# Kernel tuning notes

Measured on AMD Instinct MI355X. Metric: run time of the kernel, lower is better.

## Reference

```python
import jax, jax.numpy as jnp
import numpy as np
import math

TOP_K = 2
CAP_FACTOR = 1.25
AUX_W = 0.01


def setup_inputs() -> dict:
    key = jax.random.key(0)
    k1, k2 = jax.random.split(key)
    x = jax.random.normal(k1, (8192, 4096), dtype=jnp.float32)
    # gate weight, torch init std=0.01, stored as (E, D) like nn.Linear
    gate_w = jax.random.normal(k2, (64, 4096), dtype=jnp.float32) * 0.01
    return {"x": x, "gate_w": gate_w}


def reference(x, gate_w):
    N, D = x.shape
    E = gate_w.shape[0]
    K = TOP_K
    C = max(math.ceil(CAP_FACTOR * N / E), 1)  # expert capacity

    logits = x @ gate_w.T                      # (N, E)
    probs = jax.nn.softmax(logits, axis=-1)    # (N, E)
    vals, idx = jax.lax.top_k(probs, K)        # (N, K)
    vals = vals / vals.sum(axis=-1, keepdims=True)

    # Parallel replacement of the serial double loop: flatten (N,K) row-major
    # (token-major, then k) which matches the loop iteration order exactly.
    flat_e = idx.reshape(-1)                               # (N*K,) expert ids
    oh = jax.nn.one_hot(flat_e, E, dtype=jnp.int32)        # (N*K, E)
    # exclusive prefix count of prior assignments to each expert
    pos = jnp.cumsum(oh, axis=0) - oh                      # (N*K, E)
    slot = jnp.take_along_axis(pos, flat_e[:, None], axis=1)[:, 0]  # (N*K,)
    # In the torch loop the counter saturates at C (only incremented when
    # c < C), so slot==prior_total is equivalent: kept iff prior_total < C.
    keep = slot < C
    slot_s = jnp.where(keep, slot, 0)
    tok = jnp.arange(N * K) // K

    combine_weights = jnp.zeros((N, E, C), dtype=x.dtype).at[
        tok, flat_e, slot_s].add(jnp.where(keep, vals.reshape(-1), 0.0))
    dispatch_mask = (jnp.zeros((N, E, C), dtype=jnp.int32).at[
        tok, flat_e, slot_s].add(keep.astype(jnp.int32))) > 0

    # load balancing loss
    f = oh.astype(jnp.float32).reshape(N, K, E).mean(axis=(0, 1))  # (E,)
    p = probs.mean(axis=0)                                         # (E,)
    load_loss = AUX_W * E * jnp.sum(f * p)

    return dispatch_mask, combine_weights, probs, load_loss
```

## Files before the change

kernel.cpp:

```cpp
#include <hip/hip_runtime.h>
#include <math.h>

#define N_TOK 8192
#define DIM   4096
#define NEXP  64
#define CAP   160
#define NEC   (83886080ULL)
#define OFF_CW    (83886080ULL)
#define OFF_PROBS (167772160ULL)
#define OFF_LOSS  (168296448ULL)
#define NA    16384

__device__ __forceinline__ float wave_max64(float v) {
    for (int m = 1; m < 64; m <<= 1) v = fmaxf(v, __shfl_xor(v, m, 64));
    return v;
}
__device__ __forceinline__ float wave_sum64(float v) {
    for (int m = 1; m < 64; m <<= 1) v += __shfl_xor(v, m, 64);
    return v;
}
__device__ __forceinline__ void wave_argmax64(float& v, int& i) {
    for (int m = 1; m < 64; m <<= 1) {
        float ov = __shfl_xor(v, m, 64);
        int   oi = __shfl_xor(i, m, 64);
        if (ov > v || (ov == v && oi < i)) { v = ov; i = oi; }
    }
}

__global__ __launch_bounds__(256) void k_gemm(const float* __restrict__ x,
                                              const float* __restrict__ gw,
                                              float* __restrict__ part, int dps) {
    __shared__ float xs[64][68];
    __shared__ float wsh[64][68];
    const int tb = blockIdx.x * 64;
    const int d_begin = blockIdx.y * dps;
    const int t  = threadIdx.x;
    const int tx = t & 15, ty = t >> 4;
    float acc[4][4] = {};
    for (int ci = 0; ci < dps / 64; ++ci) {
        const int d0 = d_begin + ci * 64;
        for (int it = 0; it < 4; ++it) {
            int idx = t + 256 * it;
            int row = idx >> 4;
            int d4  = idx & 15;
            *(float4*)(&xs[row][4 * d4]) =
                *(const float4*)(x + (size_t)(tb + row) * DIM + d0 + 4 * d4);
            *(float4*)(&wsh[row][4 * d4]) =
                *(const float4*)(gw + (size_t)row * DIM + d0 + 4 * d4);
        }
        __syncthreads();
        for (int d4 = 0; d4 < 16; ++d4) {
            float4 xa[4], wb[4];
            for (int i = 0; i < 4; ++i) xa[i] = *(const float4*)(&xs[ty + 16 * i][4 * d4]);
            for (int j = 0; j < 4; ++j) wb[j] = *(const float4*)(&wsh[tx + 16 * j][4 * d4]);
            for (int i = 0; i < 4; ++i)
                for (int j = 0; j < 4; ++j) {
                    acc[i][j] = fmaf(xa[i].x, wb[j].x, acc[i][j]);
                    acc[i][j] = fmaf(xa[i].y, wb[j].y, acc[i][j]);
                    acc[i][j] = fmaf(xa[i].z, wb[j].z, acc[i][j]);
                    acc[i][j] = fmaf(xa[i].w, wb[j].w, acc[i][j]);
                }
        }
        __syncthreads();
    }
    for (int i = 0; i < 4; ++i)
        for (int j = 0; j < 4; ++j)
            part[(size_t)blockIdx.y * N_TOK * NEXP +
                 (size_t)(tb + ty + 16 * i) * NEXP + (tx + 16 * j)] = acc[i][j];
}

__global__ __launch_bounds__(256) void k_router(const float* __restrict__ part, int S,
                                                float* __restrict__ probs_out,
                                                int* __restrict__ rec_e,
                                                float* __restrict__ rec_w) {
    const int tok  = blockIdx.x * 4 + (threadIdx.x >> 6);
    const int lane = threadIdx.x & 63;
    float l = 0.f;
    for (int s = 0; s < S; ++s)
        l += part[(size_t)s * N_TOK * NEXP + (size_t)tok * NEXP + lane];
    const float m  = wave_max64(l);
    const float ex = expf(l - m);
    const float sm = wave_sum64(ex);
    const float p  = ex / sm;
    probs_out[(size_t)tok * NEXP + lane] = p;
    float v1 = p; int i1 = lane;
    wave_argmax64(v1, i1);
    float v2 = (lane == i1) ? -1.f : p; int i2 = lane;
    wave_argmax64(v2, i2);
    if (lane == 0) {
        const float denom = v1 + v2;
        rec_e[2 * tok]     = i1;
        rec_e[2 * tok + 1] = i2;
        rec_w[2 * tok]     = v1 / denom;
        rec_w[2 * tok + 1] = v2 / denom;
    }
}

__global__ __launch_bounds__(256) void k_preduce(const float* __restrict__ probs,
                                                 float* __restrict__ p_sum) {
    __shared__ float sh[256];
    const int e = threadIdx.x & 63, tg = threadIdx.x >> 6;
    const int tok0 = blockIdx.x * 1024;
    float a = 0.f;
    for (int k = 0; k < 256; ++k)
        a += probs[(size_t)(tok0 + tg + 4 * k) * NEXP + e];
    sh[threadIdx.x] = a;
    __syncthreads();
    if (threadIdx.x < 64) {
        float s = sh[threadIdx.x] + sh[64 + threadIdx.x] +
                  sh[128 + threadIdx.x] + sh[192 + threadIdx.x];
        atomicAdd(&p_sum[threadIdx.x], s);
    }
}

__global__ void k_count(const int* __restrict__ rec_e, int* __restrict__ chunk_cnt) {
    __shared__ int cnt[64];
    const int lane = threadIdx.x, b = blockIdx.x;
    cnt[lane] = 0;
    __syncthreads();
    for (int r = 0; r < 4; ++r)
        atomicAdd(&cnt[rec_e[b * 256 + r * 64 + lane]], 1);
    __syncthreads();
    chunk_cnt[b * 64 + lane] = cnt[lane];
}

__global__ void k_scan(const int* __restrict__ chunk_cnt, int* __restrict__ chunk_base,
                       const float* __restrict__ p_sum, float* __restrict__ loss_out) {
    const int e = threadIdx.x;
    int run = 0;
    for (int b = 0; b < 64; ++b) {
        chunk_base[b * 64 + e] = run;
        run += chunk_cnt[b * 64 + e];
    }
    float term = ((float)run / (float)NA) * (p_sum[e] / (float)N_TOK);
    term = wave_sum64(term);
    if (e == 0) loss_out[0] = 0.01f * 64.f * term;
}

__global__ void k_slots(const int* __restrict__ rec_e, const int* __restrict__ chunk_base,
                        int* __restrict__ rec_s) {
    __shared__ int cnt[64];
    __shared__ int she[64];
    const int lane = threadIdx.x, b = blockIdx.x;
    cnt[lane] = chunk_base[b * 64 + lane];
    __syncthreads();
    for (int r = 0; r < 4; ++r) {
        const int i = b * 256 + r * 64 + lane;
        const int e = rec_e[i];
        she[lane] = e;
        __syncthreads();
        int prior = 0, total = 0;
        for (int j = 0; j < 64; ++j) {
            int mt = (she[j] == e);
            total += mt;
            prior += (j < lane) ? mt : 0;
        }
        const int sb   = cnt[e];
        const int slot = sb + prior;
        rec_s[i] = (slot < CAP) ? slot : -1;
        __syncthreads();
        if (prior == 0) cnt[e] = sb + total;
        __syncthreads();
    }
}

__global__ __launch_bounds__(256) void k_write(const int* __restrict__ rec_e,
                                               const int* __restrict__ rec_s,
                                               const float* __restrict__ rec_w,
                                               float* __restrict__ out) {
    const int tok = blockIdx.x;
    const int e1 = rec_e[2 * tok], e2 = rec_e[2 * tok + 1];
    const int s1 = rec_s[2 * tok], s2 = rec_s[2 * tok + 1];
    const float w1 = rec_w[2 * tok], w2 = rec_w[2 * tok + 1];
    const int p1 = (s1 >= 0) ? e1 * CAP + s1 : -1;
    const int p2 = (s2 >= 0) ? e2 * CAP + s2 : -1;
    const int o1 = (p1 >= 0) ? (p1 >> 2) : -1, c1 = p1 & 3;
    const int o2 = (p2 >= 0) ? (p2 >> 2) : -1, c2 = p2 & 3;
    float* dm = out + (size_t)tok * (NEXP * CAP);
    float* cw = out + OFF_CW + (size_t)tok * (NEXP * CAP);
    for (int it = 0; it < 10; ++it) {
        const int o = it * 256 + threadIdx.x;
        float4 d = {0.f, 0.f, 0.f, 0.f};
        float4 c = {0.f, 0.f, 0.f, 0.f};
        if (o == o1) { ((float*)&d)[c1] = 1.f; ((float*)&c)[c1] = w1; }
        if (o == o2) { ((float*)&d)[c2] = 1.f; ((float*)&c)[c2] = w2; }
        *(float4*)(dm + 4 * o) = d;
        *(float4*)(cw + 4 * o) = c;
    }
}

extern "C" void kernel_launch(void* const* d_in, const int* in_sizes, int n_in,
                              void* d_out, int out_size, void* d_ws, size_t ws_size,
                              hipStream_t stream) {
    const float* x  = (const float*)d_in[0];
    const float* gw = (const float*)d_in[1];
    float* out = (float*)d_out;

    int S = 4;
    size_t need = ((size_t)S * N_TOK * NEXP + 3 * NA + 2 * 4096 + 64) * 4;
    if (ws_size < need) S = 1;
    char* w = (char*)d_ws;
    float* part      = (float*)w;
    int*   rec_e     = (int*)(w + (size_t)S * N_TOK * NEXP * 4);
    float* rec_w     = (float*)((char*)rec_e + NA * 4);
    int*   rec_s     = (int*)((char*)rec_w + NA * 4);
    int*   chunk_cnt = (int*)((char*)rec_s + NA * 4);
    int*   chunk_base= (int*)((char*)chunk_cnt + 4096 * 4);
    float* p_sum     = (float*)((char*)chunk_base + 4096 * 4);

    hipMemsetAsync(p_sum, 0, 64 * 4, stream);

    dim3 g1(128, S);
    k_gemm<<<g1, 256, 0, stream>>>(x, gw, part, DIM / S);
    k_router<<<2048, 256, 0, stream>>>(part, S, out + OFF_PROBS, rec_e, rec_w);
    k_preduce<<<8, 256, 0, stream>>>(out + OFF_PROBS, p_sum);
    k_count<<<64, 64, 0, stream>>>(rec_e, chunk_cnt);
    k_scan<<<1, 64, 0, stream>>>(chunk_cnt, chunk_base, p_sum, out + OFF_LOSS);
    k_slots<<<64, 64, 0, stream>>>(rec_e, chunk_base, rec_s);
    k_write<<<8192, 256, 0, stream>>>(rec_e, rec_s, rec_w, out);
}
```

Before: 858.9 us.

## Replace count/scan/slot kernels with per-expert ballot assignment and fuse loss into write

```diff
diff --git a/kernel.cpp b/kernel.cpp
--- a/kernel.cpp
+++ b/kernel.cpp
@@ -5,11 +5,12 @@
 #define DIM   4096
 #define NEXP  64
 #define CAP   160
-#define NEC   (83886080ULL)
 #define OFF_CW    (83886080ULL)
 #define OFF_PROBS (167772160ULL)
 #define OFF_LOSS  (168296448ULL)
 #define NA    16384
+
+typedef float vfloat4 __attribute__((ext_vector_type(4)));
 
 __device__ __forceinline__ float wave_max64(float v) {
     for (int m = 1; m < 64; m <<= 1) v = fmaxf(v, __shfl_xor(v, m, 64));
@@ -97,78 +98,59 @@
 }
 
 __global__ __launch_bounds__(256) void k_preduce(const float* __restrict__ probs,
-                                                 float* __restrict__ p_sum) {
+                                                 float* __restrict__ psum_part) {
     __shared__ float sh[256];
     const int e = threadIdx.x & 63, tg = threadIdx.x >> 6;
-    const int tok0 = blockIdx.x * 1024;
+    const int tok0 = blockIdx.x * 128;
     float a = 0.f;
-    for (int k = 0; k < 256; ++k)
+    for (int k = 0; k < 32; ++k)
         a += probs[(size_t)(tok0 + tg + 4 * k) * NEXP + e];
     sh[threadIdx.x] = a;
     __syncthreads();
-    if (threadIdx.x < 64) {
-        float s = sh[threadIdx.x] + sh[64 + threadIdx.x] +
-                  sh[128 + threadIdx.x] + sh[192 + threadIdx.x];
-        atomicAdd(&p_sum[threadIdx.x], s);
-    }
+    if (threadIdx.x < 64)
+        psum_part[blockIdx.x * 64 + threadIdx.x] =
+            sh[threadIdx.x] + sh[64 + threadIdx.x] +
+            sh[128 + threadIdx.x] + sh[192 + threadIdx.x];
 }
 
-__global__ void k_count(const int* __restrict__ rec_e, int* __restrict__ chunk_cnt) {
-    __shared__ int cnt[64];
-    const int lane = threadIdx.x, b = blockIdx.x;
-    cnt[lane] = 0;
-    __syncthreads();
-    for (int r = 0; r < 4; ++r)
-        atomicAdd(&cnt[rec_e[b * 256 + r * 64 + lane]], 1);
-    __syncthreads();
-    chunk_cnt[b * 64 + lane] = cnt[lane];
-}
-
-__global__ void k_scan(const int* __restrict__ chunk_cnt, int* __restrict__ chunk_base,
-                       const float* __restrict__ p_sum, float* __restrict__ loss_out) {
-    const int e = threadIdx.x;
-    int run = 0;
-    for (int b = 0; b < 64; ++b) {
-        chunk_base[b * 64 + e] = run;
-        run += chunk_cnt[b * 64 + e];
+__global__ __launch_bounds__(256) void k_assign(const int* __restrict__ rec_e,
+                                                int* __restrict__ rec_s,
+                                                int* __restrict__ ecnt) {
+    const int w    = blockIdx.x * 4 + (threadIdx.x >> 6);
+    const int lane = threadIdx.x & 63;
+    int base = 0;
+    const unsigned long long ltmask = (1ull << lane) - 1ull;
+    for (int c = 0; c < NA / 64; ++c) {
+        const int i = c * 64 + lane;
+        const int e = rec_e[i];
+        const unsigned long long mask = __ballot(e == w);
+        if (e == w) {
+            const int slot = base + __popcll(mask & ltmask);
+            rec_s[i] = (slot < CAP) ? slot : -1;
+        }
+        base += __popcll(mask);
     }
-    float term = ((float)run / (float)NA) * (p_sum[e] / (float)N_TOK);
-    term = wave_sum64(term);
-    if (e == 0) loss_out[0] = 0.01f * 64.f * term;
-}
-
-__global__ void k_slots(const int* __restrict__ rec_e, const int* __restrict__ chunk_base,
-                        int* __restrict__ rec_s) {
-    __shared__ int cnt[64];
-    __shared__ int she[64];
-    const int lane = threadIdx.x, b = blockIdx.x;
-    cnt[lane] = chunk_base[b * 64 + lane];
-    __syncthreads();
-    for (int r = 0; r < 4; ++r) {
-        const int i = b * 256 + r * 64 + lane;
-        const int e = rec_e[i];
-        she[lane] = e;
-        __syncthreads();
-        int prior = 0, total = 0;
-        for (int j = 0; j < 64; ++j) {
-            int mt = (she[j] == e);
-            total += mt;
-            prior += (j < lane) ? mt : 0;
-        }
-        const int sb   = cnt[e];
-        const int slot = sb + prior;
-        rec_s[i] = (slot < CAP) ? slot : -1;
-        __syncthreads();
-        if (prior == 0) cnt[e] = sb + total;
-        __syncthreads();
-    }
+    if (lane == 0) ecnt[w] = base;
 }
 
 __global__ __launch_bounds__(256) void k_write(const int* __restrict__ rec_e,
                                                const int* __restrict__ rec_s,
                                                const float* __restrict__ rec_w,
+                                               const int* __restrict__ ecnt,
+                                               const float* __restrict__ psum_part,
                                                float* __restrict__ out) {
     const int tok = blockIdx.x;
+    if (tok == N_TOK) {
+        if (threadIdx.x < 64) {
+            const int e = threadIdx.x;
+            float ps = 0.f;
+            for (int b = 0; b < 64; ++b) ps += psum_part[b * 64 + e];
+            float term = ((float)ecnt[e] / (float)NA) * (ps / (float)N_TOK);
+            term = wave_sum64(term);
+            if (e == 0) out[OFF_LOSS] = 0.01f * 64.f * term;
+        }
+        return;
+    }
     const int e1 = rec_e[2 * tok], e2 = rec_e[2 * tok + 1];
     const int s1 = rec_s[2 * tok], s2 = rec_s[2 * tok + 1];
     const float w1 = rec_w[2 * tok], w2 = rec_w[2 * tok + 1];
@@ -180,12 +162,12 @@
     float* cw = out + OFF_CW + (size_t)tok * (NEXP * CAP);
     for (int it = 0; it < 10; ++it) {
         const int o = it * 256 + threadIdx.x;
-        float4 d = {0.f, 0.f, 0.f, 0.f};
-        float4 c = {0.f, 0.f, 0.f, 0.f};
-        if (o == o1) { ((float*)&d)[c1] = 1.f; ((float*)&c)[c1] = w1; }
-        if (o == o2) { ((float*)&d)[c2] = 1.f; ((float*)&c)[c2] = w2; }
-        *(float4*)(dm + 4 * o) = d;
-        *(float4*)(cw + 4 * o) = c;
+        vfloat4 d = {0.f, 0.f, 0.f, 0.f};
+        vfloat4 c = {0.f, 0.f, 0.f, 0.f};
+        if (o == o1) { d[c1] = 1.f; c[c1] = w1; }
+        if (o == o2) { d[c2] = 1.f; c[c2] = w2; }
+        __builtin_nontemporal_store(d, (vfloat4*)(dm + 4 * o));
+        __builtin_nontemporal_store(c, (vfloat4*)(cw + 4 * o));
     }
 }
 
@@ -196,26 +178,22 @@
     const float* gw = (const float*)d_in[1];
     float* out = (float*)d_out;
 
-    int S = 4;
-    size_t need = ((size_t)S * N_TOK * NEXP + 3 * NA + 2 * 4096 + 64) * 4;
-    if (ws_size < need) S = 1;
+    int S = 8;
+    const size_t fixed = (size_t)(3 * NA + 64 * 64 + 64) * 4;
+    while (S > 1 && ws_size < (size_t)S * N_TOK * NEXP * 4 + fixed) S >>= 1;
+
     char* w = (char*)d_ws;
     float* part      = (float*)w;
     int*   rec_e     = (int*)(w + (size_t)S * N_TOK * NEXP * 4);
     float* rec_w     = (float*)((char*)rec_e + NA * 4);
     int*   rec_s     = (int*)((char*)rec_w + NA * 4);
-    int*   chunk_cnt = (int*)((char*)rec_s + NA * 4);
-    int*   chunk_base= (int*)((char*)chunk_cnt + 4096 * 4);
-    float* p_sum     = (float*)((char*)chunk_base + 4096 * 4);
-
-    hipMemsetAsync(p_sum, 0, 64 * 4, stream);
+    float* psum_part = (float*)((char*)rec_s + NA * 4);
+    int*   ecnt      = (int*)((char*)psum_part + 64 * 64 * 4);
 
     dim3 g1(128, S);
     k_gemm<<<g1, 256, 0, stream>>>(x, gw, part, DIM / S);
     k_router<<<2048, 256, 0, stream>>>(part, S, out + OFF_PROBS, rec_e, rec_w);
-    k_preduce<<<8, 256, 0, stream>>>(out + OFF_PROBS, p_sum);
-    k_count<<<64, 64, 0, stream>>>(rec_e, chunk_cnt);
-    k_scan<<<1, 64, 0, stream>>>(chunk_cnt, chunk_base, p_sum, out + OFF_LOSS);
-    k_slots<<<64, 64, 0, stream>>>(rec_e, chunk_base, rec_s);
-    k_write<<<8192, 256, 0, stream>>>(rec_e, rec_s, rec_w, out);
+    k_preduce<<<64, 256, 0, stream>>>(out + OFF_PROBS, psum_part);
+    k_assign<<<16, 256, 0, stream>>>(rec_e, rec_s, ecnt);
+    k_write<<<N_TOK + 1, 256, 0, stream>>>(rec_e, rec_s, rec_w, ecnt, psum_part, out);
 }
```

Result: no change. 864.1 us (+0.6%).
